# Performance work log

Hardware: AMD Instinct MI355X
Metric: run time of the kernel (lower is better)

Reference implementation:

```python
import jax, jax.numpy as jnp
import numpy as np

N = 50000   # nodes
E = 512000  # edges
D = 64      # embedding_dim
L = 4       # num_layers
ATOM_DIMS = np.array([119, 5, 12, 12, 10, 6, 6, 2, 2])  # OGB atom feature vocab sizes
BOND_DIMS = np.array([5, 6, 2])                          # OGB bond feature vocab sizes


def _ln(x, g, b, eps=1e-5):
    m = x.mean(-1, keepdims=True)
    v = x.var(-1, keepdims=True)
    return (x - m) * jax.lax.rsqrt(v + eps) * g + b


def setup_inputs() -> dict:
    key = jax.random.key(0)
    ks = jax.random.split(key, 12)
    s = 0.05
    x = jax.random.randint(ks[0], (N, 9), 0, jnp.asarray(ATOM_DIMS)[None, :])
    edge_attr = jax.random.randint(ks[1], (E, 3), 0, jnp.asarray(BOND_DIMS)[None, :])
    edge_index = jax.random.randint(ks[2], (2, E), 0, N)
    # padded embedding tables: [n_feats, max_vocab, D]
    atom_emb = jax.random.normal(ks[3], (9, 119, D), jnp.float32) * s
    bond_emb = jax.random.normal(ks[4], (3, 6, D), jnp.float32) * s
    eps = jnp.zeros((L,), jnp.float32)  # GIN eps, init 0
    W1 = jax.random.normal(ks[5], (L, D, 2 * D), jnp.float32) * s
    b1 = jnp.zeros((L, 2 * D), jnp.float32)
    W2 = jax.random.normal(ks[6], (L, 2 * D, D), jnp.float32) * s
    b2 = jnp.zeros((L, D), jnp.float32)
    ln_g = jnp.ones((L, D), jnp.float32)
    ln_b = jnp.zeros((L, D), jnp.float32)
    Wu1 = jax.random.normal(ks[7], (L, 3 * D, 3 * D), jnp.float32) * s
    bu1 = jnp.zeros((L, 3 * D), jnp.float32)
    ug = jnp.ones((L, 3 * D), jnp.float32)
    ub = jnp.zeros((L, 3 * D), jnp.float32)
    Wu2 = jax.random.normal(ks[8], (L, 3 * D, D), jnp.float32) * s
    bu2 = jnp.zeros((L, D), jnp.float32)
    return dict(x=x, edge_attr=edge_attr, edge_index=edge_index,
                atom_emb=atom_emb, bond_emb=bond_emb, eps=eps,
                W1=W1, b1=b1, W2=W2, b2=b2, ln_g=ln_g, ln_b=ln_b,
                Wu1=Wu1, bu1=bu1, ug=ug, ub=ub, Wu2=Wu2, bu2=bu2)


def reference(x, edge_attr, edge_index, atom_emb, bond_emb, eps,
              W1, b1, W2, b2, ln_g, ln_b, Wu1, bu1, ug, ub, Wu2, bu2):
    # Atom/Bond encoders: sum of per-column categorical embeddings
    node = atom_emb[jnp.arange(9)[None, :], x].sum(axis=1)       # [N, D]
    edge = bond_emb[jnp.arange(3)[None, :], edge_attr].sum(axis=1)  # [E, D]
    src, dst = edge_index[0], edge_index[1]
    for l in range(L):
        # MyGINConv (GINE): aggregate relu(x_src + e) at dst, mlp((1+eps)x + agg)
        msg = jax.nn.relu(node[src] + edge)                      # [E, D]
        agg = jax.ops.segment_sum(msg, dst, num_segments=N)      # [N, D]
        h = (1.0 + eps[l]) * node + agg
        h = jax.nn.relu(h @ W1[l] + b1[l]) @ W2[l] + b2[l]       # conv MLP
        h = _ln(h, ln_g[l], ln_b[l])                             # batch_norms[l] (LayerNorm)
        node = jax.nn.relu(h) + node                             # dropout=identity (eval) + residual
        # SparseEdgeUpdateLayer (residual=True)
        cat = jnp.concatenate([node[src], node[dst], edge], axis=-1)  # [E, 3D]
        m = _ln(cat @ Wu1[l] + bu1[l], ug[l], ub[l])
        edge = jax.nn.relu(m) @ Wu2[l] + bu2[l] + edge
    return node, edge
```

## Files before the change

### kernel.cpp

```cpp
#include <hip/hip_runtime.h>
#include <hip/hip_bf16.h>


#define GIN_N 50000
#define GIN_E 512000

typedef __attribute__((ext_vector_type(8))) short short8;
typedef __attribute__((ext_vector_type(4))) float f32x4;
typedef unsigned short u16;

__device__ __forceinline__ u16 bf16r(float x) {
    unsigned u = __builtin_bit_cast(unsigned, x);
    u += 0x7fffu + ((u >> 16) & 1u);
    return (u16)(u >> 16);
}
__device__ __forceinline__ float bf16f(u16 h) {
    unsigned u = ((unsigned)h) << 16;
    return __builtin_bit_cast(float, u);
}

__global__ __launch_bounds__(256) void atom_encode(const int* __restrict__ x,
        const float* __restrict__ emb, float* __restrict__ node,
        float* __restrict__ agg, int N) {
    int idx = blockIdx.x * 256 + threadIdx.x;
    int n = idx >> 6, lane = idx & 63;
    if (n >= N) return;
    float s = 0.f;
#pragma unroll
    for (int f = 0; f < 9; ++f) {
        int v = x[n * 9 + f];
        s += emb[(f * 119 + v) * 64 + lane];
    }
    size_t o = (size_t)n * 64 + lane;
    node[o] = s;
    agg[o] = 0.f;
}

__global__ __launch_bounds__(256) void bond_encode_scatter(
        const int* __restrict__ ea, const float* __restrict__ emb,
        u16* __restrict__ edgeB, const int* __restrict__ src,
        const int* __restrict__ dst, const float* __restrict__ node,
        float* __restrict__ agg, int E) {
    int idx = blockIdx.x * 256 + threadIdx.x;
    int e = idx >> 6, lane = idx & 63;
    if (e >= E) return;
    float s = 0.f;
#pragma unroll
    for (int f = 0; f < 3; ++f) {
        int v = ea[e * 3 + f];
        s += emb[(f * 6 + v) * 64 + lane];
    }
    edgeB[(size_t)e * 64 + lane] = bf16r(s);
    int si = src[e], di = dst[e];
    float msg = fmaxf(node[(size_t)si * 64 + lane] + s, 0.f);
    unsafeAtomicAdd(&agg[(size_t)di * 64 + lane], msg);
}

__global__ __launch_bounds__(256) void pack_b1(const float* __restrict__ W,
        u16* __restrict__ out, int K, int Nc, int F) {
    int tid = blockIdx.x * 256 + threadIdx.x;
    int lane = tid & 63;
    int frag = (tid >> 6) % F;
    int layer = tid / (F * 64);
    int tpr = Nc / 16;
    int ks = frag / tpr, tt = frag % tpr;
    int k0 = ks * 32 + ((lane >> 4) << 3);
    int col = tt * 16 + (lane & 15);
    const float* w = W + (size_t)layer * K * Nc;
    u16* o = out + ((size_t)layer * F + frag) * 512 + (size_t)lane * 8;
#pragma unroll
    for (int j = 0; j < 8; ++j) o[j] = bf16r(w[(size_t)(k0 + j) * Nc + col]);
}
__global__ __launch_bounds__(256) void pack_b2(const float* __restrict__ W,
        u16* __restrict__ out, int K, int Nc, int F) {
    int tid = blockIdx.x * 256 + threadIdx.x;
    int lane = tid & 63;
    int frag = (tid >> 6) % F;
    int layer = tid / (F * 64);
    int tpr = Nc / 16;
    int ks = frag / tpr, tt = frag % tpr;
    int k0 = ks * 32 + ((lane >> 4) << 3);
    int col = tt * 16 + (lane & 15);
    const float* w = W + (size_t)layer * K * Nc;
    u16* o = out + ((size_t)layer * F + frag) * 1024 + (size_t)lane * 8;
#pragma unroll
    for (int j = 0; j < 8; ++j) {
        float v = w[(size_t)(k0 + j) * Nc + col];
        u16 hi = bf16r(v);
        o[j] = hi;
        o[512 + j] = bf16r(v - bf16f(hi));
    }
}

__global__ __launch_bounds__(256, 2) void node_mlp(
        float* __restrict__ node, u16* __restrict__ nodeB,
        float* __restrict__ agg,
        const float* __restrict__ epsArr, int l,
        const u16* __restrict__ pw1, const u16* __restrict__ pw2,
        const float* __restrict__ b1, const float* __restrict__ b2,
        const float* __restrict__ lng, const float* __restrict__ lnb, int N) {
    __shared__ u16 xH[64][68], xL[64][68];
    __shared__ u16 hH[64][132], hL[64][132];
    __shared__ float pS[4][64], pS2[4][64], lnM[64], lnR[64];
    const int t = threadIdx.x, w = t >> 6, lane = t & 63;
    const int g = lane >> 4, c0 = lane & 15;
    const float epf = 1.f + epsArr[l];

#pragma unroll
    for (int i = 0; i < 16; ++i) {
        int r = w * 16 + i;
        int n = blockIdx.x * 64 + r;
        float x = 0.f;
        if (n < N) {
            size_t o = (size_t)n * 64 + lane;
            x = epf * node[o] + agg[o];
            agg[o] = 0.f;
        }
        u16 h = bf16r(x);
        xH[r][lane] = h;
        xL[r][lane] = bf16r(x - bf16f(h));
    }
    __syncthreads();

    f32x4 a1[4][2];
#pragma unroll
    for (int sp = 0; sp < 4; ++sp)
#pragma unroll
        for (int lt = 0; lt < 2; ++lt) a1[sp][lt] = (f32x4)0.f;
#pragma unroll
    for (int ks = 0; ks < 2; ++ks) {
        short8 aH[4], aL[4];
#pragma unroll
        for (int sp = 0; sp < 4; ++sp) {
            aH[sp] = *(const short8*)&xH[sp * 16 + c0][ks * 32 + g * 8];
            aL[sp] = *(const short8*)&xL[sp * 16 + c0][ks * 32 + g * 8];
        }
#pragma unroll
        for (int lt = 0; lt < 2; ++lt) {
            const u16* p = pw1 + (size_t)(ks * 8 + w * 2 + lt) * 1024 + (size_t)lane * 8;
            short8 bH = *(const short8*)p;
            short8 bL = *(const short8*)(p + 512);
#pragma unroll
            for (int sp = 0; sp < 4; ++sp) {
                a1[sp][lt] = __builtin_amdgcn_mfma_f32_16x16x32_bf16(aH[sp], bH, a1[sp][lt], 0, 0, 0);
                a1[sp][lt] = __builtin_amdgcn_mfma_f32_16x16x32_bf16(aH[sp], bL, a1[sp][lt], 0, 0, 0);
                a1[sp][lt] = __builtin_amdgcn_mfma_f32_16x16x32_bf16(aL[sp], bH, a1[sp][lt], 0, 0, 0);
            }
        }
    }
#pragma unroll
    for (int lt = 0; lt < 2; ++lt) {
        int col = w * 32 + lt * 16 + c0;
        float bias = b1[col];
#pragma unroll
        for (int sp = 0; sp < 4; ++sp)
#pragma unroll
            for (int rg = 0; rg < 4; ++rg) {
                int r = sp * 16 + g * 4 + rg;
                float v = fmaxf(a1[sp][lt][rg] + bias, 0.f);
                u16 h = bf16r(v);
                hH[r][col] = h;
                hL[r][col] = bf16r(v - bf16f(h));
            }
    }
    __syncthreads();

    f32x4 a2[4];
#pragma unroll
    for (int sp = 0; sp < 4; ++sp) a2[sp] = (f32x4)0.f;
#pragma unroll
    for (int ks = 0; ks < 4; ++ks) {
        const u16* p = pw2 + (size_t)(ks * 4 + w) * 1024 + (size_t)lane * 8;
        short8 bH = *(const short8*)p;
        short8 bL = *(const short8*)(p + 512);
#pragma unroll
        for (int sp = 0; sp < 4; ++sp) {
            short8 aH = *(const short8*)&hH[sp * 16 + c0][ks * 32 + g * 8];
            short8 aL = *(const short8*)&hL[sp * 16 + c0][ks * 32 + g * 8];
            a2[sp] = __builtin_amdgcn_mfma_f32_16x16x32_bf16(aH, bH, a2[sp], 0, 0, 0);
            a2[sp] = __builtin_amdgcn_mfma_f32_16x16x32_bf16(aH, bL, a2[sp], 0, 0, 0);
            a2[sp] = __builtin_amdgcn_mfma_f32_16x16x32_bf16(aL, bH, a2[sp], 0, 0, 0);
        }
    }
    float bias2 = b2[w * 16 + c0];
    float s1v[4][4], s2v[4][4];
#pragma unroll
    for (int sp = 0; sp < 4; ++sp)
#pragma unroll
        for (int rg = 0; rg < 4; ++rg) {
            float v = a2[sp][rg] + bias2;
            a2[sp][rg] = v;
            s1v[sp][rg] = v;
            s2v[sp][rg] = v * v;
        }
#pragma unroll
    for (int off = 1; off < 16; off <<= 1)
#pragma unroll
        for (int sp = 0; sp < 4; ++sp)
#pragma unroll
            for (int rg = 0; rg < 4; ++rg) {
                s1v[sp][rg] += __shfl_xor(s1v[sp][rg], off);
                s2v[sp][rg] += __shfl_xor(s2v[sp][rg], off);
            }
    if (c0 == 0) {
#pragma unroll
        for (int sp = 0; sp < 4; ++sp)
#pragma unroll
            for (int rg = 0; rg < 4; ++rg) {
                int r = sp * 16 + g * 4 + rg;
                pS[w][r] = s1v[sp][rg];
                pS2[w][r] = s2v[sp][rg];
            }
    }
    __syncthreads();
    if (t < 64) {
        float a = pS[0][t] + pS[1][t] + pS[2][t] + pS[3][t];
        float b = pS2[0][t] + pS2[1][t] + pS2[2][t] + pS2[3][t];
        float mean = a * (1.f / 64.f);
        float var = b * (1.f / 64.f) - mean * mean;
        lnM[t] = mean;
        lnR[t] = rsqrtf(var + 1e-5f);
    }
    __syncthreads();

    int col = w * 16 + c0;
    float gg = lng[col], bc = lnb[col];
#pragma unroll
    for (int sp = 0; sp < 4; ++sp)
#pragma unroll
        for (int rg = 0; rg < 4; ++rg) {
            int r = sp * 16 + g * 4 + rg;
            int n = blockIdx.x * 64 + r;
            if (n < N) {
                size_t o = (size_t)n * 64 + col;
                float y = (a2[sp][rg] - lnM[r]) * lnR[r] * gg + bc;
                float out = fmaxf(y, 0.f) + node[o];
                node[o] = out;
                nodeB[o] = bf16r(out);
            }
        }
}

template <bool SCATTER>
__global__ __launch_bounds__(256, 4) void edge_update_v16(
        const int* __restrict__ src, const int* __restrict__ dst,
        const float* __restrict__ node, const u16* __restrict__ nodeB,
        u16* __restrict__ edgeB, float* __restrict__ edgeF,
        float* __restrict__ agg,
        const u16* __restrict__ pb1, const u16* __restrict__ pb2,
        const float* __restrict__ bu1, const float* __restrict__ ug,
        const float* __restrict__ ub, const float* __restrict__ bu2) {
    __shared__ u16 cat[64][200];
    __shared__ float pS[4][64], pS2[4][64];
    __shared__ float lnM[64], lnR[64];
    const int t = threadIdx.x, w = t >> 6, lane = t & 63;
    const int g = lane >> 4, c0 = lane & 15;
    const long eB = (long)blockIdx.x * 64;

#pragma unroll
    for (int i = 0; i < 16; ++i) {
        int r = w * 16 + i;
        long ge = eB + r;
        int s = src[ge], d = dst[ge];
        cat[r][lane]       = nodeB[(size_t)s * 64 + lane];
        cat[r][64 + lane]  = nodeB[(size_t)d * 64 + lane];
        cat[r][128 + lane] = edgeB[(size_t)ge * 64 + lane];
    }
    __syncthreads();

    f32x4 acc[4][3];
#pragma unroll
    for (int sp = 0; sp < 4; ++sp)
#pragma unroll
        for (int lt = 0; lt < 3; ++lt) acc[sp][lt] = (f32x4)0.f;
#pragma unroll
    for (int ks = 0; ks < 6; ++ks) {
        short8 a[4];
#pragma unroll
        for (int sp = 0; sp < 4; ++sp)
            a[sp] = *(const short8*)&cat[sp * 16 + c0][ks * 32 + g * 8];
#pragma unroll
        for (int lt = 0; lt < 3; ++lt) {
            const u16* p = pb1 + (size_t)(ks * 12 + w * 3 + lt) * 512 + (size_t)lane * 8;
            short8 b = *(const short8*)p;
#pragma unroll
            for (int sp = 0; sp < 4; ++sp)
                acc[sp][lt] = __builtin_amdgcn_mfma_f32_16x16x32_bf16(a[sp], b, acc[sp][lt], 0, 0, 0);
        }
    }

    float bs[3];
#pragma unroll
    for (int lt = 0; lt < 3; ++lt) bs[lt] = bu1[w * 48 + lt * 16 + c0];
    float s1v[4][4], s2v[4][4];
#pragma unroll
    for (int sp = 0; sp < 4; ++sp)
#pragma unroll
        for (int rg = 0; rg < 4; ++rg) { s1v[sp][rg] = 0.f; s2v[sp][rg] = 0.f; }
#pragma unroll
    for (int sp = 0; sp < 4; ++sp)
#pragma unroll
        for (int lt = 0; lt < 3; ++lt)
#pragma unroll
            for (int rg = 0; rg < 4; ++rg) {
                float v = acc[sp][lt][rg] + bs[lt];
                acc[sp][lt][rg] = v;
                s1v[sp][rg] += v;
                s2v[sp][rg] += v * v;
            }
#pragma unroll
    for (int off = 1; off < 16; off <<= 1)
#pragma unroll
        for (int sp = 0; sp < 4; ++sp)
#pragma unroll
            for (int rg = 0; rg < 4; ++rg) {
                s1v[sp][rg] += __shfl_xor(s1v[sp][rg], off);
                s2v[sp][rg] += __shfl_xor(s2v[sp][rg], off);
            }
    if (c0 == 0) {
#pragma unroll
        for (int sp = 0; sp < 4; ++sp)
#pragma unroll
            for (int rg = 0; rg < 4; ++rg) {
                int r = sp * 16 + g * 4 + rg;
                pS[w][r] = s1v[sp][rg];
                pS2[w][r] = s2v[sp][rg];
            }
    }
    __syncthreads();
    if (t < 64) {
        float a = pS[0][t] + pS[1][t] + pS[2][t] + pS[3][t];
        float b = pS2[0][t] + pS2[1][t] + pS2[2][t] + pS2[3][t];
        float mean = a * (1.f / 192.f);
        float var = b * (1.f / 192.f) - mean * mean;
        lnM[t] = mean;
        lnR[t] = rsqrtf(var + 1e-5f);
    }
    __syncthreads();

#pragma unroll
    for (int lt = 0; lt < 3; ++lt) {
        int col = w * 48 + lt * 16 + c0;
        float gg = ug[col], bb = ub[col];
#pragma unroll
        for (int sp = 0; sp < 4; ++sp)
#pragma unroll
            for (int rg = 0; rg < 4; ++rg) {
                int r = sp * 16 + g * 4 + rg;
                float v = (acc[sp][lt][rg] - lnM[r]) * lnR[r] * gg + bb;
                cat[r][col] = bf16r(fmaxf(v, 0.f));
            }
    }
    __syncthreads();

    f32x4 a2[4];
#pragma unroll
    for (int sp = 0; sp < 4; ++sp) a2[sp] = (f32x4)0.f;
#pragma unroll
    for (int ks = 0; ks < 6; ++ks) {
        const u16* p = pb2 + (size_t)(ks * 4 + w) * 512 + (size_t)lane * 8;
        short8 b = *(const short8*)p;
#pragma unroll
        for (int sp = 0; sp < 4; ++sp) {
            short8 a = *(const short8*)&cat[sp * 16 + c0][ks * 32 + g * 8];
            a2[sp] = __builtin_amdgcn_mfma_f32_16x16x32_bf16(a, b, a2[sp], 0, 0, 0);
        }
    }

    const int col = w * 16 + c0;
    const float bb2 = bu2[col];
#pragma unroll
    for (int sp = 0; sp < 4; ++sp)
#pragma unroll
        for (int rg = 0; rg < 4; ++rg) {
            int r = sp * 16 + g * 4 + rg;
            long ge = eB + r;
            size_t off = (size_t)ge * 64 + col;
            float eNew = a2[sp][rg] + bb2 + bf16f(edgeB[off]);
            if (SCATTER) {
                edgeB[off] = bf16r(eNew);
                int s2 = src[ge], d2 = dst[ge];
                float msg = fmaxf(node[(size_t)s2 * 64 + col] + eNew, 0.f);
                unsafeAtomicAdd(&agg[(size_t)d2 * 64 + col], msg);
            } else {
                edgeF[off] = eNew;
            }
        }
}

extern "C" void kernel_launch(void* const* d_in, const int* in_sizes, int n_in,
                              void* d_out, int out_size, void* d_ws, size_t ws_size,
                              hipStream_t stream) {
    const int*   x         = (const int*)d_in[0];
    const int*   edge_attr = (const int*)d_in[1];
    const int*   edge_index= (const int*)d_in[2];
    const float* atom_emb  = (const float*)d_in[3];
    const float* bond_emb  = (const float*)d_in[4];
    const float* eps       = (const float*)d_in[5];
    const float* W1        = (const float*)d_in[6];
    const float* b1        = (const float*)d_in[7];
    const float* W2        = (const float*)d_in[8];
    const float* b2        = (const float*)d_in[9];
    const float* ln_g      = (const float*)d_in[10];
    const float* ln_b      = (const float*)d_in[11];
    const float* Wu1       = (const float*)d_in[12];
    const float* bu1       = (const float*)d_in[13];
    const float* ug        = (const float*)d_in[14];
    const float* ub        = (const float*)d_in[15];
    const float* Wu2       = (const float*)d_in[16];
    const float* bu2       = (const float*)d_in[17];

    const int N = GIN_N, E = GIN_E;
    const int* src = edge_index;
    const int* dst = edge_index + E;

    float* node  = (float*)d_out;
    float* edgeF = (float*)d_out + (size_t)N * 64;

    char* ws = (char*)d_ws;
    float* agg   = (float*)ws;  ws += (size_t)N * 64 * 4;
    u16*   nodeB = (u16*)ws;    ws += (size_t)N * 64 * 2;
    u16*   edgeB = (u16*)ws;    ws += (size_t)E * 64 * 2;
    u16* pb1     = (u16*)ws;    ws += (size_t)4 * 72 * 512 * 2;
    u16* pb2     = (u16*)ws;    ws += (size_t)4 * 24 * 512 * 2;
    u16* pw1     = (u16*)ws;    ws += (size_t)4 * 16 * 1024 * 2;
    u16* pw2     = (u16*)ws;    ws += (size_t)4 * 16 * 1024 * 2;

    pack_b1<<<(4 * 72 * 64) / 256, 256, 0, stream>>>(Wu1, pb1, 192, 192, 72);
    pack_b1<<<(4 * 24 * 64) / 256, 256, 0, stream>>>(Wu2, pb2, 192, 64, 24);
    pack_b2<<<(4 * 16 * 64) / 256, 256, 0, stream>>>(W1, pw1, 64, 128, 16);
    pack_b2<<<(4 * 16 * 64) / 256, 256, 0, stream>>>(W2, pw2, 128, 64, 16);

    atom_encode<<<(N * 64 + 255) / 256, 256, 0, stream>>>(x, atom_emb, node, agg, N);
    bond_encode_scatter<<<(E * 64) / 256, 256, 0, stream>>>(edge_attr, bond_emb,
        edgeB, src, dst, node, agg, E);

    const int nodeBlocks = (N + 63) / 64;
    for (int l = 0; l < 4; ++l) {
        node_mlp<<<nodeBlocks, 256, 0, stream>>>(node, nodeB, agg, eps, l,
            pw1 + (size_t)l * 16 * 1024, pw2 + (size_t)l * 16 * 1024,
            b1 + (size_t)l * 128, b2 + (size_t)l * 64,
            ln_g + (size_t)l * 64, ln_b + (size_t)l * 64, N);
        if (l < 3)
            edge_update_v16<true><<<E / 64, 256, 0, stream>>>(src, dst, node, nodeB,
                edgeB, edgeF, agg,
                pb1 + (size_t)l * 72 * 512, pb2 + (size_t)l * 24 * 512,
                bu1 + (size_t)l * 192,
                ug + (size_t)l * 192, ub + (size_t)l * 192,
                bu2 + (size_t)l * 64);
        else
            edge_update_v16<false><<<E / 64, 256, 0, stream>>>(src, dst, node, nodeB,
                edgeB, edgeF, agg,
                pb1 + (size_t)l * 72 * 512, pb2 + (size_t)l * 24 * 512,
                bu1 + (size_t)l * 192,
                ug + (size_t)l * 192, ub + (size_t)l * 192,
                bu2 + (size_t)l * 64);
    }
}
```

Measured before the change: 881.8 us.

## Give each wave its own 16-edge row slab in edge update to drop block syncs

The edge-update kernel now has each wave own 16 rows (edges) across all 192 hidden columns, instead of splitting columns across waves. The LayerNorm row statistics can then be reduced entirely with in-wave shuffles, and the shared-memory partial sums and all `__syncthreads` barriers go away. The src/dst index reloads in the scatter epilogue are also hoisted per row. The cost is that every wave must now stream the full packed weight matrices, roughly four times more weight fetches per block from cache.

Result: slower. 1.015 ms (+15.1%).

```diff
diff --git a/kernel.cpp b/kernel.cpp
--- a/kernel.cpp
+++ b/kernel.cpp
@@ -242,7 +242,7 @@
 }
 
 template <bool SCATTER>
-__global__ __launch_bounds__(256, 4) void edge_update_v16(
+__global__ __launch_bounds__(256, 4) void edge_update_v17(
         const int* __restrict__ src, const int* __restrict__ dst,
         const float* __restrict__ node, const u16* __restrict__ nodeB,
         u16* __restrict__ edgeB, float* __restrict__ edgeF,
@@ -251,8 +251,6 @@
         const float* __restrict__ bu1, const float* __restrict__ ug,
         const float* __restrict__ ub, const float* __restrict__ bu2) {
     __shared__ u16 cat[64][200];
-    __shared__ float pS[4][64], pS2[4][64];
-    __shared__ float lnM[64], lnR[64];
     const int t = threadIdx.x, w = t >> 6, lane = t & 63;
     const int g = lane >> 4, c0 = lane & 15;
     const long eB = (long)blockIdx.x * 64;
@@ -266,126 +264,94 @@
         cat[r][64 + lane]  = nodeB[(size_t)d * 64 + lane];
         cat[r][128 + lane] = edgeB[(size_t)ge * 64 + lane];
     }
-    __syncthreads();
-
-    f32x4 acc[4][3];
-#pragma unroll
-    for (int sp = 0; sp < 4; ++sp)
-#pragma unroll
-        for (int lt = 0; lt < 3; ++lt) acc[sp][lt] = (f32x4)0.f;
+
+    f32x4 acc[12];
+#pragma unroll
+    for (int lt = 0; lt < 12; ++lt) acc[lt] = (f32x4)0.f;
 #pragma unroll
     for (int ks = 0; ks < 6; ++ks) {
-        short8 a[4];
-#pragma unroll
-        for (int sp = 0; sp < 4; ++sp)
-            a[sp] = *(const short8*)&cat[sp * 16 + c0][ks * 32 + g * 8];
-#pragma unroll
-        for (int lt = 0; lt < 3; ++lt) {
-            const u16* p = pb1 + (size_t)(ks * 12 + w * 3 + lt) * 512 + (size_t)lane * 8;
+        short8 a = *(const short8*)&cat[w * 16 + c0][ks * 32 + g * 8];
+#pragma unroll
+        for (int lt = 0; lt < 12; ++lt) {
+            const u16* p = pb1 + (size_t)(ks * 12 + lt) * 512 + (size_t)lane * 8;
             short8 b = *(const short8*)p;
-#pragma unroll
-            for (int sp = 0; sp < 4; ++sp)
-                acc[sp][lt] = __builtin_amdgcn_mfma_f32_16x16x32_bf16(a[sp], b, acc[sp][lt], 0, 0, 0);
-        }
-    }
-
-    float bs[3];
-#pragma unroll
-    for (int lt = 0; lt < 3; ++lt) bs[lt] = bu1[w * 48 + lt * 16 + c0];
-    float s1v[4][4], s2v[4][4];
-#pragma unroll
-    for (int sp = 0; sp < 4; ++sp)
-#pragma unroll
-        for (int rg = 0; rg < 4; ++rg) { s1v[sp][rg] = 0.f; s2v[sp][rg] = 0.f; }
-#pragma unroll
-    for (int sp = 0; sp < 4; ++sp)
-#pragma unroll
-        for (int lt = 0; lt < 3; ++lt)
-#pragma unroll
-            for (int rg = 0; rg < 4; ++rg) {
-                float v = acc[sp][lt][rg] + bs[lt];
-                acc[sp][lt][rg] = v;
-                s1v[sp][rg] += v;
-                s2v[sp][rg] += v * v;
-            }
+            acc[lt] = __builtin_amdgcn_mfma_f32_16x16x32_bf16(a, b, acc[lt], 0, 0, 0);
+        }
+    }
+
+    float s1[4] = {0.f, 0.f, 0.f, 0.f}, s2[4] = {0.f, 0.f, 0.f, 0.f};
+#pragma unroll
+    for (int lt = 0; lt < 12; ++lt) {
+        float bias = bu1[lt * 16 + c0];
+#pragma unroll
+        for (int rg = 0; rg < 4; ++rg) {
+            float v = acc[lt][rg] + bias;
+            acc[lt][rg] = v;
+            s1[rg] += v;
+            s2[rg] += v * v;
+        }
+    }
 #pragma unroll
     for (int off = 1; off < 16; off <<= 1)
 #pragma unroll
-        for (int sp = 0; sp < 4; ++sp)
-#pragma unroll
-            for (int rg = 0; rg < 4; ++rg) {
-                s1v[sp][rg] += __shfl_xor(s1v[sp][rg], off);
-                s2v[sp][rg] += __shfl_xor(s2v[sp][rg], off);
-            }
-    if (c0 == 0) {
-#pragma unroll
-        for (int sp = 0; sp < 4; ++sp)
-#pragma unroll
-            for (int rg = 0; rg < 4; ++rg) {
-                int r = sp * 16 + g * 4 + rg;
-                pS[w][r] = s1v[sp][rg];
-                pS2[w][r] = s2v[sp][rg];
-            }
-    }
-    __syncthreads();
-    if (t < 64) {
-        float a = pS[0][t] + pS[1][t] + pS[2][t] + pS[3][t];
-        float b = pS2[0][t] + pS2[1][t] + pS2[2][t] + pS2[3][t];
-        float mean = a * (1.f / 192.f);
-        float var = b * (1.f / 192.f) - mean * mean;
-        lnM[t] = mean;
-        lnR[t] = rsqrtf(var + 1e-5f);
-    }
-    __syncthreads();
-
-#pragma unroll
-    for (int lt = 0; lt < 3; ++lt) {
-        int col = w * 48 + lt * 16 + c0;
+        for (int rg = 0; rg < 4; ++rg) {
+            s1[rg] += __shfl_xor(s1[rg], off);
+            s2[rg] += __shfl_xor(s2[rg], off);
+        }
+    float mean[4], rs[4];
+#pragma unroll
+    for (int rg = 0; rg < 4; ++rg) {
+        mean[rg] = s1[rg] * (1.f / 192.f);
+        float var = s2[rg] * (1.f / 192.f) - mean[rg] * mean[rg];
+        rs[rg] = rsqrtf(var + 1e-5f);
+    }
+
+#pragma unroll
+    for (int lt = 0; lt < 12; ++lt) {
+        int col = lt * 16 + c0;
         float gg = ug[col], bb = ub[col];
 #pragma unroll
-        for (int sp = 0; sp < 4; ++sp)
-#pragma unroll
-            for (int rg = 0; rg < 4; ++rg) {
-                int r = sp * 16 + g * 4 + rg;
-                float v = (acc[sp][lt][rg] - lnM[r]) * lnR[r] * gg + bb;
-                cat[r][col] = bf16r(fmaxf(v, 0.f));
-            }
-    }
-    __syncthreads();
+        for (int rg = 0; rg < 4; ++rg) {
+            int r = w * 16 + g * 4 + rg;
+            float v = (acc[lt][rg] - mean[rg]) * rs[rg] * gg + bb;
+            cat[r][col] = bf16r(fmaxf(v, 0.f));
+        }
+    }
 
     f32x4 a2[4];
 #pragma unroll
-    for (int sp = 0; sp < 4; ++sp) a2[sp] = (f32x4)0.f;
+    for (int lt = 0; lt < 4; ++lt) a2[lt] = (f32x4)0.f;
 #pragma unroll
     for (int ks = 0; ks < 6; ++ks) {
-        const u16* p = pb2 + (size_t)(ks * 4 + w) * 512 + (size_t)lane * 8;
-        short8 b = *(const short8*)p;
-#pragma unroll
-        for (int sp = 0; sp < 4; ++sp) {
-            short8 a = *(const short8*)&cat[sp * 16 + c0][ks * 32 + g * 8];
-            a2[sp] = __builtin_amdgcn_mfma_f32_16x16x32_bf16(a, b, a2[sp], 0, 0, 0);
-        }
-    }
-
-    const int col = w * 16 + c0;
-    const float bb2 = bu2[col];
-#pragma unroll
-    for (int sp = 0; sp < 4; ++sp)
-#pragma unroll
-        for (int rg = 0; rg < 4; ++rg) {
-            int r = sp * 16 + g * 4 + rg;
-            long ge = eB + r;
+        short8 a = *(const short8*)&cat[w * 16 + c0][ks * 32 + g * 8];
+#pragma unroll
+        for (int lt = 0; lt < 4; ++lt) {
+            const u16* p = pb2 + (size_t)(ks * 4 + lt) * 512 + (size_t)lane * 8;
+            short8 b = *(const short8*)p;
+            a2[lt] = __builtin_amdgcn_mfma_f32_16x16x32_bf16(a, b, a2[lt], 0, 0, 0);
+        }
+    }
+
+#pragma unroll
+    for (int rg = 0; rg < 4; ++rg) {
+        int r = w * 16 + g * 4 + rg;
+        long ge = eB + r;
+        int s2i = 0, d2i = 0;
+        if (SCATTER) { s2i = src[ge]; d2i = dst[ge]; }
+#pragma unroll
+        for (int lt = 0; lt < 4; ++lt) {
+            int col = lt * 16 + c0;
             size_t off = (size_t)ge * 64 + col;
-            float eNew = a2[sp][rg] + bb2 + bf16f(edgeB[off]);
+            float eNew = a2[lt][rg] + bu2[col] + bf16f(edgeB[off]);
             if (SCATTER) {
                 edgeB[off] = bf16r(eNew);
-                int s2 = src[ge], d2 = dst[ge];
-                float msg = fmaxf(node[(size_t)s2 * 64 + col] + eNew, 0.f);
-                unsafeAtomicAdd(&agg[(size_t)d2 * 64 + col], msg);
+                float msg = fmaxf(node[(size_t)s2i * 64 + col] + eNew, 0.f);
+                unsafeAtomicAdd(&agg[(size_t)d2i * 64 + col], msg);
             } else {
                 edgeF[off] = eNew;
             }
         }
+    }
 }
 
 extern "C" void kernel_launch(void* const* d_in, const int* in_sizes, int n_in,
@@ -442,14 +408,14 @@
             b1 + (size_t)l * 128, b2 + (size_t)l * 64,
             ln_g + (size_t)l * 64, ln_b + (size_t)l * 64, N);
         if (l < 3)
-            edge_update_v16<true><<<E / 64, 256, 0, stream>>>(src, dst, node, nodeB,
+            edge_update_v17<true><<<E / 64, 256, 0, stream>>>(src, dst, node, nodeB,
                 edgeB, edgeF, agg,
                 pb1 + (size_t)l * 72 * 512, pb2 + (size_t)l * 24 * 512,
                 bu1 + (size_t)l * 192,
                 ug + (size_t)l * 192, ub + (size_t)l * 192,
                 bu2 + (size_t)l * 64);
         else
-            edge_update_v16<false><<<E / 64, 256, 0, stream>>>(src, dst, node, nodeB,
+            edge_update_v17<false><<<E / 64, 256, 0, stream>>>(src, dst, node, nodeB,
                 edgeB, edgeF, agg,
                 pb1 + (size_t)l * 72 * 512, pb2 + (size_t)l * 24 * 512,
                 bu1 + (size_t)l * 192,
```
